# Optimization experiments

Measured on AMD Instinct MI355X. Metric: run time of the kernel, lower is better.

The kernel has to match this reference:

```python
import jax, jax.numpy as jnp
import numpy as np

N_NODES = 50000


def _gcn_layer(x, src, dst, W, b, n_nodes):
    # PyG GCNConv: h = x @ W, add self-loops, sym-normalized scatter-add, + bias
    h = x @ W  # [N, Dout]
    loop = jnp.arange(n_nodes, dtype=src.dtype)
    src2 = jnp.concatenate([src, loop])
    dst2 = jnp.concatenate([dst, loop])
    ones = jnp.ones(src2.shape[0], dtype=x.dtype)
    deg = jax.ops.segment_sum(ones, dst2, num_segments=n_nodes)  # in-degree w/ self-loops
    dinv = jnp.where(deg > 0, jax.lax.rsqrt(deg), 0.0)
    norm = dinv[src2] * dinv[dst2]  # [E+N]
    msg = h[src2] * norm[:, None]   # gather + scale
    out = jax.ops.segment_sum(msg, dst2, num_segments=n_nodes)  # scatter-add
    return out + b


def setup_inputs() -> dict:
    key = jax.random.key(0)
    k1, k2, k3, k4 = jax.random.split(key, 4)
    x = jax.random.normal(k1, (N_NODES, 128), dtype=jnp.float32)
    edge_index = jax.random.randint(k2, (2, 500000), 0, N_NODES, dtype=jnp.int64)
    W1 = jax.random.normal(k3, (128, 128), dtype=jnp.float32) * (1.0 / np.sqrt(128))
    b1 = jnp.zeros((128,), dtype=jnp.float32)
    W2 = jax.random.normal(k4, (128, 64), dtype=jnp.float32) * (1.0 / np.sqrt(128))
    b2 = jnp.zeros((64,), dtype=jnp.float32)
    return {"x": x, "edge_index": edge_index, "W1": W1, "b1": b1, "W2": W2, "b2": b2}


def reference(x, edge_index, W1, b1, W2, b2):
    src, dst = edge_index[0], edge_index[1]
    n = x.shape[0]
    h = _gcn_layer(x, src, dst, W1, b1, n)
    h = jax.nn.relu(h)
    out = _gcn_layer(h, src, dst, W2, b2, n)
    return out
```

## Files before the change

### kernel.cpp

```cpp
#include <hip/hip_runtime.h>
#include <hip/hip_bf16.h>
#include <cstddef>


typedef __attribute__((ext_vector_type(8))) short short8;
typedef __attribute__((ext_vector_type(4))) float f32x4;
typedef unsigned long long u64;

__device__ inline unsigned short f2bf(float f) {
    __hip_bfloat16 b = __float2bfloat16(f);
    return *reinterpret_cast<unsigned short*>(&b);
}
__device__ inline float bf2f_lo(unsigned int u) {
    unsigned int v = u << 16;
    return *reinterpret_cast<float*>(&v);
}
__device__ inline float bf2f_hi(unsigned int u) {
    unsigned int v = u & 0xffff0000u;
    return *reinterpret_cast<float*>(&v);
}
__device__ inline u64 ld_acq64(u64* p) {
    return __hip_atomic_load(p, __ATOMIC_ACQUIRE, __HIP_MEMORY_SCOPE_AGENT);
}
__device__ inline void st_rel64(u64* p, u64 v) {
    __hip_atomic_store(p, v, __ATOMIC_RELEASE, __HIP_MEMORY_SCOPE_AGENT);
}

__global__ __launch_bounds__(256) void count_kernel(const int* __restrict__ dst, int E,
                                                    int* __restrict__ deg,
                                                    unsigned short* __restrict__ rank,
                                                    const float* __restrict__ W1,
                                                    const float* __restrict__ W2,
                                                    unsigned short* __restrict__ W1f,
                                                    unsigned short* __restrict__ W2f,
                                                    u64* __restrict__ lb, int CB) {
    int b = blockIdx.x;
    int tid = threadIdx.x;
    if (b >= CB) {
        int idx = (b - CB) * 256 + tid;
        if (idx < 64) lb[idx] = 0;
        if (idx < 3072) {
            const float* W;
            unsigned short* Wf;
            int n, oct, Nc;
            if (idx < 2048) { W = W1; Wf = W1f; Nc = 128; n = idx >> 4; oct = idx & 15; }
            else { W = W2; Wf = W2f; Nc = 64; int i2 = idx - 2048; n = i2 >> 4; oct = i2 & 15; }
            int k0 = oct * 8;
            int ks = k0 >> 5, quad = (k0 >> 3) & 3, ntg = n >> 4;
            short8 v;
            #pragma unroll
            for (int j = 0; j < 8; j++) v[j] = (short)f2bf(W[(k0 + j) * Nc + n]);
            int off = (((ntg * 4 + ks) * 64) + (n & 15) + 16 * quad) * 8;
            *(short8*)(Wf + off) = v;
        }
        return;
    }
    int i = (b * 256 + tid) * 4;
    if (i + 3 < E) {
        int4 d = *(const int4*)(dst + i);
        unsigned short r0 = (unsigned short)atomicAdd(&deg[d.x], 1);
        unsigned short r1 = (unsigned short)atomicAdd(&deg[d.y], 1);
        unsigned short r2 = (unsigned short)atomicAdd(&deg[d.z], 1);
        unsigned short r3 = (unsigned short)atomicAdd(&deg[d.w], 1);
        *(ushort4*)(rank + i) = make_ushort4(r0, r1, r2, r3);
    } else {
        for (; i < E; i++) rank[i] = (unsigned short)atomicAdd(&deg[dst[i]], 1);
    }
}

__global__ __launch_bounds__(256) void scan_lb_kernel(const int* __restrict__ deg, int N,
                                                      u64* __restrict__ lb,
                                                      int* __restrict__ offs,
                                                      float* __restrict__ dinv) {
    __shared__ int ws[4];
    __shared__ int s_prefix;
    int tid = threadIdx.x;
    int sb = blockIdx.x;
    int SB = gridDim.x;
    int lane = tid & 63;
    int wv = tid >> 6;

    int i = sb * 1024 + tid * 4;
    int v0 = (i + 0 < N) ? deg[i + 0] : 0;
    int v1 = (i + 1 < N) ? deg[i + 1] : 0;
    int v2 = (i + 2 < N) ? deg[i + 2] : 0;
    int v3 = (i + 3 < N) ? deg[i + 3] : 0;
    int tsum = v0 + v1 + v2 + v3;
    int xs = tsum;
    #pragma unroll
    for (int off = 1; off < 64; off <<= 1) {
        int y = __shfl_up(xs, off, 64);
        if (lane >= off) xs += y;
    }
    if (lane == 63) ws[wv] = xs;
    __syncthreads();
    int wprefix = 0;
    #pragma unroll
    for (int w2 = 0; w2 < 4; w2++) wprefix += (w2 < wv) ? ws[w2] : 0;
    int chunk_total = ws[0] + ws[1] + ws[2] + ws[3];

    if (wv == 0) {
        if (lane == 0)
            st_rel64(&lb[sb], ((u64)(unsigned)chunk_total << 2) | 1ull);
        int contrib = 0;
        if (sb > 0) {
            int pred = sb - 1 - lane;
            for (;;) {
                u64 v = (pred >= 0) ? ld_acq64(&lb[pred]) : 2ull;
                int flag = (int)(v & 3);
                u64 ball2 = __ballot(flag == 2);
                u64 ball0 = __ballot(flag == 0);
                if (ball2 != 0) {
                    int L = __ffsll(ball2) - 1;
                    if ((ball0 & ((1ull << L) - 1)) == 0) {
                        contrib = (lane <= L) ? (int)(unsigned)(v >> 2) : 0;
                        break;
                    }
                }
                __builtin_amdgcn_s_sleep(1);
            }
            #pragma unroll
            for (int off = 32; off >= 1; off >>= 1)
                contrib += __shfl_xor(contrib, off, 64);
        }
        if (lane == 0) {
            st_rel64(&lb[sb], ((u64)(unsigned)(contrib + chunk_total) << 2) | 2ull);
            s_prefix = contrib;
        }
    }
    __syncthreads();

    int carry = s_prefix;
    int e0 = carry + wprefix + xs - tsum;
    int e1 = e0 + v0, e2 = e1 + v1, e3 = e2 + v2;
    if (i + 0 < N) { offs[i + 0] = e0; dinv[i + 0] = rsqrtf((float)(v0 + 1)); }
    if (i + 1 < N) { offs[i + 1] = e1; dinv[i + 1] = rsqrtf((float)(v1 + 1)); }
    if (i + 2 < N) { offs[i + 2] = e2; dinv[i + 2] = rsqrtf((float)(v2 + 1)); }
    if (i + 3 < N) { offs[i + 3] = e3; dinv[i + 3] = rsqrtf((float)(v3 + 1)); }
    if (sb == SB - 1 && tid == 0) offs[N] = carry + chunk_total;
}

__global__ __launch_bounds__(256) void fillgemm_kernel(
    const float* __restrict__ x, const unsigned short* __restrict__ W1f,
    unsigned short* __restrict__ h1, int N,
    const int* __restrict__ src, const int* __restrict__ dst, int E,
    const int* __restrict__ offs, const unsigned short* __restrict__ rank,
    const float* __restrict__ dinv, int* __restrict__ csr) {

    const int FB = (E + 255) / 256;
    int b = blockIdx.x;
    int tid = threadIdx.x;

    __shared__ unsigned short As[64 * 128];
    __shared__ float sdinv[64];

    if (b < FB) {
        int i = b * 256 + tid;
        if (i < E) {
            int s = src[i];
            int d = dst[i];
            int pos = offs[d] + (int)rank[i];
            csr[pos] = s;
        }
        return;
    }

    constexpr int K = 128, BN = 128;
    int lane = tid & 63;
    int w = tid >> 6;
    int row0 = (b - FB) * 64;

    if (tid < 64) {
        int gr = row0 + tid;
        sdinv[tid] = (gr < N) ? dinv[gr] : 0.f;
    }

    short8 bfr[2][4];
    #pragma unroll
    for (int nl = 0; nl < 2; nl++)
        #pragma unroll
        for (int ks = 0; ks < 4; ks++)
            bfr[nl][ks] = *(const short8*)(W1f + ((((w * 2 + nl) * 4 + ks) * 64) + lane) * 8);

    #pragma unroll
    for (int it = 0; it < 8; it++) {
        int idx = it * 256 + tid;
        int row = idx >> 5, kq = idx & 31;
        int k0 = kq * 4;
        int ks = k0 >> 5, quad = (k0 >> 3) & 3, j0 = k0 & 7, mt = row >> 4;
        ushort4 o = make_ushort4(0, 0, 0, 0);
        int gr = row0 + row;
        if (gr < N) {
            float4 a = *(const float4*)(x + (size_t)gr * K + k0);
            o.x = f2bf(a.x); o.y = f2bf(a.y); o.z = f2bf(a.z); o.w = f2bf(a.w);
        }
        int off = (((mt * 4 + ks) * 64) + (row & 15) + 16 * quad) * 8 + j0;
        *(ushort4*)(As + off) = o;
    }
    __syncthreads();

    f32x4 acc[4][2];
    #pragma unroll
    for (int mt = 0; mt < 4; mt++)
        #pragma unroll
        for (int nl = 0; nl < 2; nl++) acc[mt][nl] = (f32x4){0.f, 0.f, 0.f, 0.f};

    #pragma unroll
    for (int ks = 0; ks < 4; ks++) {
        short8 af[4];
        #pragma unroll
        for (int mt = 0; mt < 4; mt++)
            af[mt] = *(const short8*)(As + (((mt * 4 + ks) * 64) + lane) * 8);
        #pragma unroll
        for (int mt = 0; mt < 4; mt++)
            #pragma unroll
            for (int nl = 0; nl < 2; nl++)
                acc[mt][nl] = __builtin_amdgcn_mfma_f32_16x16x32_bf16(
                    af[mt], bfr[nl][ks], acc[mt][nl], 0, 0, 0);
    }

    int col16 = lane & 15;
    int rowq = lane >> 4;
    #pragma unroll
    for (int mt = 0; mt < 4; mt++) {
        #pragma unroll
        for (int nl = 0; nl < 2; nl++) {
            int gc = (w * 2 + nl) * 16 + col16;
            #pragma unroll
            for (int r = 0; r < 4; r++) {
                int lr = mt * 16 + rowq * 4 + r;
                int gr = row0 + lr;
                if (gr < N) h1[(size_t)gr * BN + gc] = f2bf(acc[mt][nl][r] * sdinv[lr]);
            }
        }
    }
}

__global__ __launch_bounds__(256) void aggmm_kernel(const unsigned short* __restrict__ h1,
                                                    const int* __restrict__ offs,
                                                    const int* __restrict__ csr,
                                                    const float* __restrict__ dinv,
                                                    const float* __restrict__ b1,
                                                    const unsigned short* __restrict__ W2f,
                                                    unsigned short* __restrict__ h2,
                                                    int n) {
    __shared__ unsigned short As[4 * 64 * 8];

    int tid = threadIdx.x;
    int t = tid & 63;
    int w = tid >> 6;
    int p = t >> 5;
    int t5 = t & 31;
    int nodebase = blockIdx.x * 16;
    int node0 = nodebase + w * 4;

    int ov = offs[min(node0 + min(t, 4), n)];
    int e0a[4], dega[4], nba[4], cidx[4];
    float dia[4];
    #pragma unroll
    for (int i = 0; i < 4; i++) {
        e0a[i] = __shfl(ov, i, 64);
        dega[i] = __shfl(ov, i + 1, 64) - e0a[i];
        nba[i] = min(dega[i], 64);
        int ce = e0a[i] + min(t, max(dega[i] - 1, 0));
        cidx[i] = (dega[i] > 0) ? csr[ce] : 0;
        int node = node0 + i;
        dia[i] = (node < n) ? dinv[node] : 0.f;
    }

    short8 bw[4];
    #pragma unroll
    for (int ks = 0; ks < 4; ks++)
        bw[ks] = *(const short8*)(W2f + (((w * 4 + ks) * 64) + t) * 8);

    float4 bias = *(const float4*)(b1 + t5 * 4);

    #pragma unroll
    for (int i = 0; i < 4; i++) {
        int row16 = w * 4 + i;
        int node = node0 + i;
        float a0 = 0.f, a1 = 0.f, a2 = 0.f, a3 = 0.f;
        if (node < n) {
            if (p == 0) {
                uint2 su = *(const uint2*)(h1 + (size_t)node * 128 + t5 * 4);
                a0 = bf2f_lo(su.x); a1 = bf2f_hi(su.x);
                a2 = bf2f_lo(su.y); a3 = bf2f_hi(su.y);
            }
            for (int jb = 0; jb < nba[i]; jb += 4) {
                uint2 hu[2];
                float wv[2];
                #pragma unroll
                for (int j = 0; j < 2; j++) {
                    int ee = jb + j * 2 + p;
                    int ec = min(ee, nba[i] - 1);
                    int s = __shfl(cidx[i], ec, 64);
                    wv[j] = (ee < nba[i]) ? 1.f : 0.f;
                    hu[j] = *(const uint2*)(h1 + (size_t)s * 128 + t5 * 4);
                }
                #pragma unroll
                for (int j = 0; j < 2; j++) {
                    a0 += bf2f_lo(hu[j].x) * wv[j]; a1 += bf2f_hi(hu[j].x) * wv[j];
                    a2 += bf2f_lo(hu[j].y) * wv[j]; a3 += bf2f_hi(hu[j].y) * wv[j];
                }
            }
            int e1 = e0a[i] + dega[i];
            for (int eb = e0a[i] + 64; eb < e1; eb += 4) {
                #pragma unroll
                for (int j = 0; j < 2; j++) {
                    int ee = eb + j * 2 + p;
                    int ec = min(ee, e1 - 1);
                    int s = csr[ec];
                    float wgt = (ee < e1) ? 1.f : 0.f;
                    uint2 hu = *(const uint2*)(h1 + (size_t)s * 128 + t5 * 4);
                    a0 += bf2f_lo(hu.x) * wgt; a1 += bf2f_hi(hu.x) * wgt;
                    a2 += bf2f_lo(hu.y) * wgt; a3 += bf2f_hi(hu.y) * wgt;
                }
            }
        }
        a0 += __shfl_xor(a0, 32, 64);
        a1 += __shfl_xor(a1, 32, 64);
        a2 += __shfl_xor(a2, 32, 64);
        a3 += __shfl_xor(a3, 32, 64);
        if (p == 0) {
            if (node < n) {
                a0 = fmaxf(a0 * dia[i] + bias.x, 0.f);
                a1 = fmaxf(a1 * dia[i] + bias.y, 0.f);
                a2 = fmaxf(a2 * dia[i] + bias.z, 0.f);
                a3 = fmaxf(a3 * dia[i] + bias.w, 0.f);
            }
            int k0 = t5 * 4;
            int ks = k0 >> 5, quad = (k0 >> 3) & 3, j0 = k0 & 7;
            ushort4 pk4 = make_ushort4(f2bf(a0), f2bf(a1), f2bf(a2), f2bf(a3));
            *(ushort4*)(As + ((ks * 64) + row16 + 16 * quad) * 8 + j0) = pk4;
        }
    }
    __syncthreads();

    f32x4 acc = (f32x4){0.f, 0.f, 0.f, 0.f};
    #pragma unroll
    for (int ks = 0; ks < 4; ks++) {
        short8 af = *(const short8*)(As + ((ks * 64) + t) * 8);
        acc = __builtin_amdgcn_mfma_f32_16x16x32_bf16(af, bw[ks], acc, 0, 0, 0);
    }

    int col = w * 16 + (t & 15);
    int rowq = t >> 4;
    #pragma unroll
    for (int r = 0; r < 4; r++) {
        int gr = nodebase + rowq * 4 + r;
        if (gr < n) h2[(size_t)gr * 64 + col] = f2bf(acc[r] * dinv[gr]);
    }
}

__global__ __launch_bounds__(256) void aggout_kernel(const unsigned short* __restrict__ h2,
                                                     const int* __restrict__ offs,
                                                     const int* __restrict__ csr,
                                                     const float* __restrict__ dinv,
                                                     const float* __restrict__ b2,
                                                     float* __restrict__ out, int n) {
    int tid = threadIdx.x;
    int t = tid & 63;
    int w = tid >> 6;
    int node = blockIdx.x * 4 + w;
    if (node >= n) return;
    int p = t >> 4;
    int t4 = t & 15;

    int e0 = offs[node];
    int e1 = offs[node + 1];
    int deg = e1 - e0;
    int nb = min(deg, 64);
    int cidx = (deg > 0) ? csr[e0 + min(t, max(deg - 1, 0))] : 0;

    float a0 = 0.f, a1 = 0.f, a2 = 0.f, a3 = 0.f;
    float di = dinv[node];
    if (p == 0) {
        uint2 su = *(const uint2*)(h2 + (size_t)node * 64 + t4 * 4);
        a0 = bf2f_lo(su.x); a1 = bf2f_hi(su.x);
        a2 = bf2f_lo(su.y); a3 = bf2f_hi(su.y);
    }

    for (int jb = 0; jb < nb; jb += 8) {
        #pragma unroll
        for (int j = 0; j < 2; j++) {
            int ee = jb + j * 4 + p;
            int ec = min(ee, nb - 1);
            int s = __shfl(cidx, ec, 64);
            float wgt = (ee < deg) ? 1.f : 0.f;
            uint2 hu = *(const uint2*)(h2 + (size_t)s * 64 + t4 * 4);
            a0 += bf2f_lo(hu.x) * wgt; a1 += bf2f_hi(hu.x) * wgt;
            a2 += bf2f_lo(hu.y) * wgt; a3 += bf2f_hi(hu.y) * wgt;
        }
    }
    for (int eb = e0 + 64; eb < e1; eb += 8) {
        #pragma unroll
        for (int j = 0; j < 2; j++) {
            int ee = eb + j * 4 + p;
            int ec = min(ee, e1 - 1);
            int s = csr[ec];
            float wgt = (ee < e1) ? 1.f : 0.f;
            uint2 hu = *(const uint2*)(h2 + (size_t)s * 64 + t4 * 4);
            a0 += bf2f_lo(hu.x) * wgt; a1 += bf2f_hi(hu.x) * wgt;
            a2 += bf2f_lo(hu.y) * wgt; a3 += bf2f_hi(hu.y) * wgt;
        }
    }
    a0 += __shfl_xor(a0, 16, 64); a1 += __shfl_xor(a1, 16, 64);
    a2 += __shfl_xor(a2, 16, 64); a3 += __shfl_xor(a3, 16, 64);
    a0 += __shfl_xor(a0, 32, 64); a1 += __shfl_xor(a1, 32, 64);
    a2 += __shfl_xor(a2, 32, 64); a3 += __shfl_xor(a3, 32, 64);
    if (p == 0) {
        float4 bb = *(const float4*)(b2 + t4 * 4);
        *(float4*)(out + (size_t)node * 64 + t4 * 4) =
            make_float4(a0 * di + bb.x, a1 * di + bb.y, a2 * di + bb.z, a3 * di + bb.w);
    }
}

extern "C" void kernel_launch(void* const* d_in, const int* in_sizes, int n_in,
                              void* d_out, int out_size, void* d_ws, size_t ws_size,
                              hipStream_t stream) {
    const float* x  = (const float*)d_in[0];
    const int*   ei = (const int*)d_in[1];
    const float* W1 = (const float*)d_in[2];
    const float* b1 = (const float*)d_in[3];
    const float* W2 = (const float*)d_in[4];
    const float* b2 = (const float*)d_in[5];

    const int N = in_sizes[0] / 128;
    const int E = in_sizes[1] / 2;
    const int* src = ei;
    const int* dst = ei + E;

    char* p = (char*)d_ws;
    auto alloc = [&](size_t bytes) {
        char* r = p;
        p += (bytes + 255) & ~(size_t)255;
        return r;
    };
    int*   degi  = (int*)  alloc((size_t)N * 4);
    float* dinv  = (float*)alloc((size_t)N * 4);
    int*   offs  = (int*)  alloc((size_t)(N + 1) * 4);
    u64*   lb    = (u64*)  alloc((size_t)64 * 8);
    unsigned short* rank = (unsigned short*)alloc((size_t)E * 2);
    int*            csr  = (int*)alloc((size_t)E * 4);
    unsigned short* W1f  = (unsigned short*)alloc((size_t)128 * 128 * 2);
    unsigned short* W2f  = (unsigned short*)alloc((size_t)64 * 128 * 2);
    unsigned short* h1   = (unsigned short*)alloc((size_t)N * 128 * 2);
    unsigned short* h2   = (unsigned short*)alloc((size_t)N * 64 * 2);
    float* out = (float*)d_out;

    const int GB = (N + 63) / 64;
    const int FB = (E + 255) / 256;
    const int SB = (N + 1023) / 1024;
    const int CB = (E / 4 + 255) / 256;

    hipMemsetAsync(degi, 0, (size_t)N * 4, stream);
    count_kernel<<<CB + 12, 256, 0, stream>>>(dst, E, degi, rank,
                                              W1, W2, W1f, W2f, lb, CB);
    scan_lb_kernel<<<SB, 256, 0, stream>>>(degi, N, lb, offs, dinv);
    fillgemm_kernel<<<FB + GB, 256, 0, stream>>>(x, W1f, h1, N, src, dst, E,
                                                 offs, rank, dinv, csr);
    aggmm_kernel<<<(N + 15) / 16, 256, 0, stream>>>(h1, offs, csr, dinv, b1, W2f, h2, N);
    aggout_kernel<<<(N + 3) / 4, 256, 0, stream>>>(h2, offs, csr, dinv, b2, out, N);
}
```

Before: 173.0 us.

## Move layer-1 GEMM into count kernel and apply source dinv during aggregation

The X·W1 GEMM now runs in the same launch as the degree-count atomics instead of alongside the CSR fill. Because dinv is not yet known at that point, the source-side normalization moves into the layer-1 aggregation, which gathers dinv per neighbour through shuffles or loads. The memset is replaced by a zeroing kernel, the fill kernel handles four edges per thread, and the aggregation loops are unrolled to eight edges. This overlaps the GEMM with the atomic counting, at the cost of extra dinv gathers and per-edge multiplies in aggmm.

New measurement: 173.1 us. About the same (+0.1%).

```diff
diff --git a/kernel.cpp b/kernel.cpp
--- a/kernel.cpp
+++ b/kernel.cpp
@@ -26,45 +26,128 @@
     __hip_atomic_store(p, v, __ATOMIC_RELEASE, __HIP_MEMORY_SCOPE_AGENT);
 }
 
-__global__ __launch_bounds__(256) void count_kernel(const int* __restrict__ dst, int E,
-                                                    int* __restrict__ deg,
-                                                    unsigned short* __restrict__ rank,
-                                                    const float* __restrict__ W1,
-                                                    const float* __restrict__ W2,
-                                                    unsigned short* __restrict__ W1f,
-                                                    unsigned short* __restrict__ W2f,
-                                                    u64* __restrict__ lb, int CB) {
+__global__ __launch_bounds__(256) void init_kernel(int* __restrict__ deg, int N,
+                                                   const float* __restrict__ W1,
+                                                   const float* __restrict__ W2,
+                                                   unsigned short* __restrict__ W1f,
+                                                   unsigned short* __restrict__ W2f,
+                                                   u64* __restrict__ lb, int ZB) {
     int b = blockIdx.x;
     int tid = threadIdx.x;
-    if (b >= CB) {
-        int idx = (b - CB) * 256 + tid;
-        if (idx < 64) lb[idx] = 0;
-        if (idx < 3072) {
-            const float* W;
-            unsigned short* Wf;
-            int n, oct, Nc;
-            if (idx < 2048) { W = W1; Wf = W1f; Nc = 128; n = idx >> 4; oct = idx & 15; }
-            else { W = W2; Wf = W2f; Nc = 64; int i2 = idx - 2048; n = i2 >> 4; oct = i2 & 15; }
-            int k0 = oct * 8;
-            int ks = k0 >> 5, quad = (k0 >> 3) & 3, ntg = n >> 4;
-            short8 v;
+    if (b < ZB) {
+        int i = (b * 256 + tid) * 4;
+        if (i + 3 < N) *(int4*)(deg + i) = make_int4(0, 0, 0, 0);
+        else for (; i < N; i++) deg[i] = 0;
+        return;
+    }
+    int idx = (b - ZB) * 256 + tid;
+    if (idx < 64) lb[idx] = 0;
+    if (idx < 3072) {
+        const float* W;
+        unsigned short* Wf;
+        int n, oct, Nc;
+        if (idx < 2048) { W = W1; Wf = W1f; Nc = 128; n = idx >> 4; oct = idx & 15; }
+        else { W = W2; Wf = W2f; Nc = 64; int i2 = idx - 2048; n = i2 >> 4; oct = i2 & 15; }
+        int k0 = oct * 8;
+        int ks = k0 >> 5, quad = (k0 >> 3) & 3, ntg = n >> 4;
+        short8 v;
+        #pragma unroll
+        for (int j = 0; j < 8; j++) v[j] = (short)f2bf(W[(k0 + j) * Nc + n]);
+        int off = (((ntg * 4 + ks) * 64) + (n & 15) + 16 * quad) * 8;
+        *(short8*)(Wf + off) = v;
+    }
+}
+
+__global__ __launch_bounds__(256) void countgemm_kernel(
+    const int* __restrict__ dst, int E,
+    int* __restrict__ deg, unsigned short* __restrict__ rank,
+    const unsigned short* __restrict__ W1f,
+    const float* __restrict__ x, unsigned short* __restrict__ h1,
+    int N, int CB) {
+
+    int b = blockIdx.x;
+    int tid = threadIdx.x;
+
+    __shared__ unsigned short As[64 * 128];
+
+    if (b < CB) {
+        int i = (b * 256 + tid) * 4;
+        if (i + 3 < E) {
+            int4 d = *(const int4*)(dst + i);
+            unsigned short r0 = (unsigned short)atomicAdd(&deg[d.x], 1);
+            unsigned short r1 = (unsigned short)atomicAdd(&deg[d.y], 1);
+            unsigned short r2 = (unsigned short)atomicAdd(&deg[d.z], 1);
+            unsigned short r3 = (unsigned short)atomicAdd(&deg[d.w], 1);
+            *(ushort4*)(rank + i) = make_ushort4(r0, r1, r2, r3);
+        } else {
+            for (; i < E; i++) rank[i] = (unsigned short)atomicAdd(&deg[dst[i]], 1);
+        }
+        return;
+    }
+
+    constexpr int K = 128, BN = 128;
+    int lane = tid & 63;
+    int w = tid >> 6;
+    int row0 = (b - CB) * 64;
+
+    short8 bfr[2][4];
+    #pragma unroll
+    for (int nl = 0; nl < 2; nl++)
+        #pragma unroll
+        for (int ks = 0; ks < 4; ks++)
+            bfr[nl][ks] = *(const short8*)(W1f + ((((w * 2 + nl) * 4 + ks) * 64) + lane) * 8);
+
+    #pragma unroll
+    for (int it = 0; it < 8; it++) {
+        int idx = it * 256 + tid;
+        int row = idx >> 5, kq = idx & 31;
+        int k0 = kq * 4;
+        int ks = k0 >> 5, quad = (k0 >> 3) & 3, j0 = k0 & 7, mt = row >> 4;
+        ushort4 o = make_ushort4(0, 0, 0, 0);
+        int gr = row0 + row;
+        if (gr < N) {
+            float4 a = *(const float4*)(x + (size_t)gr * K + k0);
+            o.x = f2bf(a.x); o.y = f2bf(a.y); o.z = f2bf(a.z); o.w = f2bf(a.w);
+        }
+        int off = (((mt * 4 + ks) * 64) + (row & 15) + 16 * quad) * 8 + j0;
+        *(ushort4*)(As + off) = o;
+    }
+    __syncthreads();
+
+    f32x4 acc[4][2];
+    #pragma unroll
+    for (int mt = 0; mt < 4; mt++)
+        #pragma unroll
+        for (int nl = 0; nl < 2; nl++) acc[mt][nl] = (f32x4){0.f, 0.f, 0.f, 0.f};
+
+    #pragma unroll
+    for (int ks = 0; ks < 4; ks++) {
+        short8 af[4];
+        #pragma unroll
+        for (int mt = 0; mt < 4; mt++)
+            af[mt] = *(const short8*)(As + (((mt * 4 + ks) * 64) + lane) * 8);
+        #pragma unroll
+        for (int mt = 0; mt < 4; mt++)
             #pragma unroll
-            for (int j = 0; j < 8; j++) v[j] = (short)f2bf(W[(k0 + j) * Nc + n]);
-            int off = (((ntg * 4 + ks) * 64) + (n & 15) + 16 * quad) * 8;
-            *(short8*)(Wf + off) = v;
-        }
-        return;
-    }
-    int i = (b * 256 + tid) * 4;
-    if (i + 3 < E) {
-        int4 d = *(const int4*)(dst + i);
-        unsigned short r0 = (unsigned short)atomicAdd(&deg[d.x], 1);
-        unsigned short r1 = (unsigned short)atomicAdd(&deg[d.y], 1);
-        unsigned short r2 = (unsigned short)atomicAdd(&deg[d.z], 1);
-        unsigned short r3 = (unsigned short)atomicAdd(&deg[d.w], 1);
-        *(ushort4*)(rank + i) = make_ushort4(r0, r1, r2, r3);
-    } else {
-        for (; i < E; i++) rank[i] = (unsigned short)atomicAdd(&deg[dst[i]], 1);
+            for (int nl = 0; nl < 2; nl++)
+                acc[mt][nl] = __builtin_amdgcn_mfma_f32_16x16x32_bf16(
+                    af[mt], bfr[nl][ks], acc[mt][nl], 0, 0, 0);
+    }
+
+    int col16 = lane & 15;
+    int rowq = lane >> 4;
+    #pragma unroll
+    for (int mt = 0; mt < 4; mt++) {
+        #pragma unroll
+        for (int nl = 0; nl < 2; nl++) {
+            int gc = (w * 2 + nl) * 16 + col16;
+            #pragma unroll
+            for (int r = 0; r < 4; r++) {
+                int lr = mt * 16 + rowq * 4 + r;
+                int gr = row0 + lr;
+                if (gr < N) h1[(size_t)gr * BN + gc] = f2bf(acc[mt][nl][r]);
+            }
+        }
     }
 }
 
@@ -140,99 +223,21 @@
     if (sb == SB - 1 && tid == 0) offs[N] = carry + chunk_total;
 }
 
-__global__ __launch_bounds__(256) void fillgemm_kernel(
-    const float* __restrict__ x, const unsigned short* __restrict__ W1f,
-    unsigned short* __restrict__ h1, int N,
+__global__ __launch_bounds__(256) void fill_kernel(
     const int* __restrict__ src, const int* __restrict__ dst, int E,
     const int* __restrict__ offs, const unsigned short* __restrict__ rank,
-    const float* __restrict__ dinv, int* __restrict__ csr) {
-
-    const int FB = (E + 255) / 256;
-    int b = blockIdx.x;
-    int tid = threadIdx.x;
-
-    __shared__ unsigned short As[64 * 128];
-    __shared__ float sdinv[64];
-
-    if (b < FB) {
-        int i = b * 256 + tid;
-        if (i < E) {
-            int s = src[i];
-            int d = dst[i];
-            int pos = offs[d] + (int)rank[i];
-            csr[pos] = s;
-        }
-        return;
-    }
-
-    constexpr int K = 128, BN = 128;
-    int lane = tid & 63;
-    int w = tid >> 6;
-    int row0 = (b - FB) * 64;
-
-    if (tid < 64) {
-        int gr = row0 + tid;
-        sdinv[tid] = (gr < N) ? dinv[gr] : 0.f;
-    }
-
-    short8 bfr[2][4];
-    #pragma unroll
-    for (int nl = 0; nl < 2; nl++)
-        #pragma unroll
-        for (int ks = 0; ks < 4; ks++)
-            bfr[nl][ks] = *(const short8*)(W1f + ((((w * 2 + nl) * 4 + ks) * 64) + lane) * 8);
-
-    #pragma unroll
-    for (int it = 0; it < 8; it++) {
-        int idx = it * 256 + tid;
-        int row = idx >> 5, kq = idx & 31;
-        int k0 = kq * 4;
-        int ks = k0 >> 5, quad = (k0 >> 3) & 3, j0 = k0 & 7, mt = row >> 4;
-        ushort4 o = make_ushort4(0, 0, 0, 0);
-        int gr = row0 + row;
-        if (gr < N) {
-            float4 a = *(const float4*)(x + (size_t)gr * K + k0);
-            o.x = f2bf(a.x); o.y = f2bf(a.y); o.z = f2bf(a.z); o.w = f2bf(a.w);
-        }
-        int off = (((mt * 4 + ks) * 64) + (row & 15) + 16 * quad) * 8 + j0;
-        *(ushort4*)(As + off) = o;
-    }
-    __syncthreads();
-
-    f32x4 acc[4][2];
-    #pragma unroll
-    for (int mt = 0; mt < 4; mt++)
-        #pragma unroll
-        for (int nl = 0; nl < 2; nl++) acc[mt][nl] = (f32x4){0.f, 0.f, 0.f, 0.f};
-
-    #pragma unroll
-    for (int ks = 0; ks < 4; ks++) {
-        short8 af[4];
-        #pragma unroll
-        for (int mt = 0; mt < 4; mt++)
-            af[mt] = *(const short8*)(As + (((mt * 4 + ks) * 64) + lane) * 8);
-        #pragma unroll
-        for (int mt = 0; mt < 4; mt++)
-            #pragma unroll
-            for (int nl = 0; nl < 2; nl++)
-                acc[mt][nl] = __builtin_amdgcn_mfma_f32_16x16x32_bf16(
-                    af[mt], bfr[nl][ks], acc[mt][nl], 0, 0, 0);
-    }
-
-    int col16 = lane & 15;
-    int rowq = lane >> 4;
-    #pragma unroll
-    for (int mt = 0; mt < 4; mt++) {
-        #pragma unroll
-        for (int nl = 0; nl < 2; nl++) {
-            int gc = (w * 2 + nl) * 16 + col16;
-            #pragma unroll
-            for (int r = 0; r < 4; r++) {
-                int lr = mt * 16 + rowq * 4 + r;
-                int gr = row0 + lr;
-                if (gr < N) h1[(size_t)gr * BN + gc] = f2bf(acc[mt][nl][r] * sdinv[lr]);
-            }
-        }
+    int* __restrict__ csr) {
+    int i = (blockIdx.x * 256 + threadIdx.x) * 4;
+    if (i + 3 < E) {
+        int4 s4 = *(const int4*)(src + i);
+        int4 d4 = *(const int4*)(dst + i);
+        ushort4 r4 = *(const ushort4*)(rank + i);
+        csr[offs[d4.x] + (int)r4.x] = s4.x;
+        csr[offs[d4.y] + (int)r4.y] = s4.y;
+        csr[offs[d4.z] + (int)r4.z] = s4.z;
+        csr[offs[d4.w] + (int)r4.w] = s4.w;
+    } else {
+        for (; i < E; i++) csr[offs[dst[i]] + (int)rank[i]] = src[i];
     }
 }
 
@@ -256,14 +261,16 @@
 
     int ov = offs[min(node0 + min(t, 4), n)];
     int e0a[4], dega[4], nba[4], cidx[4];
-    float dia[4];
+    float cdw[4], dia[4];
     #pragma unroll
     for (int i = 0; i < 4; i++) {
         e0a[i] = __shfl(ov, i, 64);
         dega[i] = __shfl(ov, i + 1, 64) - e0a[i];
         nba[i] = min(dega[i], 64);
         int ce = e0a[i] + min(t, max(dega[i] - 1, 0));
-        cidx[i] = (dega[i] > 0) ? csr[ce] : 0;
+        bool has = dega[i] > 0;
+        cidx[i] = has ? csr[ce] : 0;
+        cdw[i] = has ? dinv[cidx[i]] : 0.f;
         int node = node0 + i;
         dia[i] = (node < n) ? dinv[node] : 0.f;
     }
@@ -283,34 +290,30 @@
         if (node < n) {
             if (p == 0) {
                 uint2 su = *(const uint2*)(h1 + (size_t)node * 128 + t5 * 4);
-                a0 = bf2f_lo(su.x); a1 = bf2f_hi(su.x);
-                a2 = bf2f_lo(su.y); a3 = bf2f_hi(su.y);
-            }
-            for (int jb = 0; jb < nba[i]; jb += 4) {
-                uint2 hu[2];
-                float wv[2];
+                a0 = bf2f_lo(su.x) * dia[i]; a1 = bf2f_hi(su.x) * dia[i];
+                a2 = bf2f_lo(su.y) * dia[i]; a3 = bf2f_hi(su.y) * dia[i];
+            }
+            for (int jb = 0; jb < nba[i]; jb += 8) {
                 #pragma unroll
-                for (int j = 0; j < 2; j++) {
+                for (int j = 0; j < 4; j++) {
                     int ee = jb + j * 2 + p;
                     int ec = min(ee, nba[i] - 1);
                     int s = __shfl(cidx[i], ec, 64);
-                    wv[j] = (ee < nba[i]) ? 1.f : 0.f;
-                    hu[j] = *(const uint2*)(h1 + (size_t)s * 128 + t5 * 4);
+                    float wraw = __shfl(cdw[i], ec, 64);
+                    float wgt = (ee < nba[i]) ? wraw : 0.f;
+                    uint2 hu = *(const uint2*)(h1 + (size_t)s * 128 + t5 * 4);
+                    a0 += bf2f_lo(hu.x) * wgt; a1 += bf2f_hi(hu.x) * wgt;
+                    a2 += bf2f_lo(hu.y) * wgt; a3 += bf2f_hi(hu.y) * wgt;
                 }
+            }
+            int e1 = e0a[i] + dega[i];
+            for (int eb = e0a[i] + 64; eb < e1; eb += 8) {
                 #pragma unroll
-                for (int j = 0; j < 2; j++) {
-                    a0 += bf2f_lo(hu[j].x) * wv[j]; a1 += bf2f_hi(hu[j].x) * wv[j];
-                    a2 += bf2f_lo(hu[j].y) * wv[j]; a3 += bf2f_hi(hu[j].y) * wv[j];
-                }
-            }
-            int e1 = e0a[i] + dega[i];
-            for (int eb = e0a[i] + 64; eb < e1; eb += 4) {
-                #pragma unroll
-                for (int j = 0; j < 2; j++) {
+                for (int j = 0; j < 4; j++) {
                     int ee = eb + j * 2 + p;
                     int ec = min(ee, e1 - 1);
                     int s = csr[ec];
-                    float wgt = (ee < e1) ? 1.f : 0.f;
+                    float wgt = (ee < e1) ? dinv[s] : 0.f;
                     uint2 hu = *(const uint2*)(h1 + (size_t)s * 128 + t5 * 4);
                     a0 += bf2f_lo(hu.x) * wgt; a1 += bf2f_hi(hu.x) * wgt;
                     a2 += bf2f_lo(hu.y) * wgt; a3 += bf2f_hi(hu.y) * wgt;
@@ -449,16 +452,16 @@
     float* out = (float*)d_out;
 
     const int GB = (N + 63) / 64;
-    const int FB = (E + 255) / 256;
     const int SB = (N + 1023) / 1024;
     const int CB = (E / 4 + 255) / 256;
-
-    hipMemsetAsync(degi, 0, (size_t)N * 4, stream);
-    count_kernel<<<CB + 12, 256, 0, stream>>>(dst, E, degi, rank,
-                                              W1, W2, W1f, W2f, lb, CB);
+    const int ZB = (N + 1023) / 1024;
+    const int FB4 = (E / 4 + 255) / 256;
+
+    init_kernel<<<ZB + 12, 256, 0, stream>>>(degi, N, W1, W2, W1f, W2f, lb, ZB);
+    countgemm_kernel<<<CB + GB, 256, 0, stream>>>(dst, E, degi, rank, W1f,
+                                                  x, h1, N, CB);
     scan_lb_kernel<<<SB, 256, 0, stream>>>(degi, N, lb, offs, dinv);
-    fillgemm_kernel<<<FB + GB, 256, 0, stream>>>(x, W1f, h1, N, src, dst, E,
-                                                 offs, rank, dinv, csr);
+    fill_kernel<<<FB4, 256, 0, stream>>>(src, dst, E, offs, rank, csr);
     aggmm_kernel<<<(N + 15) / 16, 256, 0, stream>>>(h1, offs, csr, dinv, b1, W2f, h2, N);
     aggout_kernel<<<(N + 3) / 4, 256, 0, stream>>>(h2, offs, csr, dinv, b2, out, N);
 }
```
